# Kernel tuning notes

Hardware: AMD Instinct MI355X
Metric: run time of the kernel (lower is better)

Reference implementation:

```python
import jax, jax.numpy as jnp
import numpy as np

N, E = 50000, 640000
D_IN, D_OUT, N_BASES = 128, 128, 8


def setup_inputs() -> dict:
    key = jax.random.key(0)
    k1, k2, k3, k4, k5, k6 = jax.random.split(key, 6)
    x = jax.random.normal(k1, (N, D_IN), dtype=jnp.float32)
    edge_index = jax.random.randint(k2, (2, E), 0, N, dtype=jnp.int64)
    # basis-decomposed relation weights (num_relations=1)
    bases = jax.random.normal(k3, (N_BASES, D_IN, D_OUT), dtype=jnp.float32) * 0.05
    comp = jax.random.normal(k4, (1, N_BASES), dtype=jnp.float32)
    root = jax.random.normal(k5, (D_IN, D_OUT), dtype=jnp.float32) * 0.05
    bias = jax.random.normal(k6, (D_OUT,), dtype=jnp.float32) * 0.01
    return {"x": x, "edge_index": edge_index, "bases": bases,
            "comp": comp, "root": root, "bias": bias}


def reference(x, edge_index, bases, comp, root, bias):
    # W[rel=0] = sum_b comp[0,b] * bases[b]  -> [D_IN, D_OUT]
    W = jnp.einsum('b,bio->io', comp[0], bases)
    src = edge_index[0]  # message sources (x_j)
    dst = edge_index[1]  # aggregation targets
    # gather -> scatter-add (aggr='add'), then relation-specific transform
    agg = jax.ops.segment_sum(x[src], dst, num_segments=x.shape[0])  # [N, D_IN]
    out = agg @ W + x @ root + bias  # root/self-loop transform + bias
    return out
```

## Files before the change

### kernel.cpp

```cpp
#include <hip/hip_runtime.h>

#define N_NODES 50000
#define N_EDGES 640000
#define D 128
#define NB 8
#define PAD 64
#define BM 64
#define LDA 136

typedef _Float16 half_t;
typedef __attribute__((ext_vector_type(8))) _Float16 half8;
typedef __attribute__((ext_vector_type(4))) float f32x4;

__device__ __forceinline__ void add4(float4& acc, const float4& v) {
    acc.x += v.x; acc.y += v.y; acc.z += v.z; acc.w += v.w;
}

__global__ __launch_bounds__(256)
void compute_Wt_kernel(const float* __restrict__ bases,
                       const float* __restrict__ comp,
                       const float* __restrict__ root,
                       half_t* __restrict__ Wt,
                       half_t* __restrict__ Rt) {
    int idx = blockIdx.x * 256 + threadIdx.x;
    if (idx >= D * D) return;
    int i = idx >> 7, o = idx & 127;
    float acc = 0.f;
#pragma unroll
    for (int b = 0; b < NB; ++b)
        acc += comp[b] * bases[((size_t)b * D + i) * D + o];
    Wt[o * D + i] = (half_t)acc;
    Rt[o * D + i] = (half_t)root[idx];
}

__global__ __launch_bounds__(256)
void zero_cnt_kernel(int* __restrict__ cnt) {
    int i = blockIdx.x * 256 + threadIdx.x;
    if (i < N_NODES) cnt[i] = 0;
}

__global__ __launch_bounds__(256)
void gemm_mfma_kernel(const float* __restrict__ x,
                      const half_t* __restrict__ Wt,
                      const half_t* __restrict__ Rt,
                      const float* __restrict__ bias,
                      half_t* __restrict__ y,
                      float* __restrict__ out) {
    __shared__ __align__(16) half_t As[BM * LDA];
    const int row0 = blockIdx.x * BM;
    const int tid  = threadIdx.x;

    {
        int r  = tid >> 2;
        int cc = (tid & 3) * 32;
        if (row0 + r < N_NODES) {
            const float4* x4 = (const float4*)x;
            size_t base = (size_t)(row0 + r) * 32 + (cc >> 2);
#pragma unroll
            for (int u = 0; u < 4; ++u) {
                float4 v0 = x4[base + 2 * u];
                float4 v1 = x4[base + 2 * u + 1];
                half8 h;
                h[0] = (half_t)v0.x; h[1] = (half_t)v0.y;
                h[2] = (half_t)v0.z; h[3] = (half_t)v0.w;
                h[4] = (half_t)v1.x; h[5] = (half_t)v1.y;
                h[6] = (half_t)v1.z; h[7] = (half_t)v1.w;
                *(half8*)&As[r * LDA + cc + u * 8] = h;
            }
        }
    }
    __syncthreads();

    const int wave = tid >> 6;
    const int lane = tid & 63;
    const int m    = lane & 15;
    const int quad = lane >> 4;

    half8 a[4];
#pragma unroll
    for (int kk = 0; kk < 4; ++kk)
        a[kk] = *(const half8*)&As[(wave * 16 + m) * LDA + kk * 32 + quad * 8];

    f32x4 accW[8], accR[8];
#pragma unroll
    for (int nt = 0; nt < 8; ++nt) {
        accW[nt] = (f32x4){0.f, 0.f, 0.f, 0.f};
        accR[nt] = (f32x4){0.f, 0.f, 0.f, 0.f};
    }

#pragma unroll
    for (int nt = 0; nt < 8; ++nt) {
        const half_t* wp = Wt + (nt * 16 + m) * D + quad * 8;
        const half_t* rp = Rt + (nt * 16 + m) * D + quad * 8;
        half8 bw[4], br[4];
#pragma unroll
        for (int kk = 0; kk < 4; ++kk) {
            bw[kk] = *(const half8*)(wp + kk * 32);
            br[kk] = *(const half8*)(rp + kk * 32);
        }
#pragma unroll
        for (int kk = 0; kk < 4; ++kk) {
            accW[nt] = __builtin_amdgcn_mfma_f32_16x16x32_f16(a[kk], bw[kk], accW[nt], 0, 0, 0);
            accR[nt] = __builtin_amdgcn_mfma_f32_16x16x32_f16(a[kk], br[kk], accR[nt], 0, 0, 0);
        }
    }

#pragma unroll
    for (int nt = 0; nt < 8; ++nt) {
        int col = nt * 16 + m;
        float bb = bias[col];
#pragma unroll
        for (int r = 0; r < 4; ++r) {
            int row = row0 + wave * 16 + quad * 4 + r;
            if (row < N_NODES) {
                y[(size_t)row * D + col]   = (half_t)accW[nt][r];
                out[(size_t)row * D + col] = accR[nt][r] + bb;
            }
        }
    }
}

__global__ __launch_bounds__(256)
void bucket_kernel(const int* __restrict__ eidx,
                   const half_t* __restrict__ y,
                   float* __restrict__ out,
                   int* __restrict__ cnt,
                   int* __restrict__ bucket) {
    int e = blockIdx.x * 256 + threadIdx.x;
    if (e >= N_EDGES) return;
    int src = eidx[e];
    int dst = eidx[N_EDGES + e];
    int pos = atomicAdd(&cnt[dst], 1);
    if (pos < PAD) {
        bucket[(size_t)dst * PAD + pos] = src;
    } else {
        const half_t* yr = y + (size_t)src * D;
        float* op = out + (size_t)dst * D;
        for (int q = 0; q < D; ++q) atomicAdd(op + q, (float)yr[q]);
    }
}

__global__ __launch_bounds__(256)
void gather_kernel(const int* __restrict__ cnt,
                   const int* __restrict__ bucket,
                   const half_t* __restrict__ y,
                   float* __restrict__ out) {
    int node = blockIdx.x * 16 + (threadIdx.x >> 4);
    int q = threadIdx.x & 15;
    if (node >= N_NODES) return;
    int c = cnt[node];
    if (c > PAD) c = PAD;
    const int* b = bucket + (size_t)node * PAD;
    float acc[8] = {0.f, 0.f, 0.f, 0.f, 0.f, 0.f, 0.f, 0.f};
    int i = 0;
    for (; i + 4 <= c; i += 4) {
        int4 s = *(const int4*)(b + i);
        half8 v0 = *(const half8*)(y + (size_t)s.x * D + q * 8);
        half8 v1 = *(const half8*)(y + (size_t)s.y * D + q * 8);
        half8 v2 = *(const half8*)(y + (size_t)s.z * D + q * 8);
        half8 v3 = *(const half8*)(y + (size_t)s.w * D + q * 8);
#pragma unroll
        for (int j = 0; j < 8; ++j)
            acc[j] += (float)v0[j] + (float)v1[j] + (float)v2[j] + (float)v3[j];
    }
    for (; i < c; ++i) {
        half8 v = *(const half8*)(y + (size_t)b[i] * D + q * 8);
#pragma unroll
        for (int j = 0; j < 8; ++j) acc[j] += (float)v[j];
    }
    float4* op = (float4*)(out + (size_t)node * D + q * 8);
    float4 o0 = op[0], o1 = op[1];
    o0.x += acc[0]; o0.y += acc[1]; o0.z += acc[2]; o0.w += acc[3];
    o1.x += acc[4]; o1.y += acc[5]; o1.z += acc[6]; o1.w += acc[7];
    op[0] = o0; op[1] = o1;
}

extern "C" void kernel_launch(void* const* d_in, const int* in_sizes, int n_in,
                              void* d_out, int out_size, void* d_ws, size_t ws_size,
                              hipStream_t stream) {
    const float* x     = (const float*)d_in[0];
    const int*   eidx  = (const int*)d_in[1];
    const float* bases = (const float*)d_in[2];
    const float* comp  = (const float*)d_in[3];
    const float* root  = (const float*)d_in[4];
    const float* bias  = (const float*)d_in[5];
    float* out = (float*)d_out;

    char* ws = (char*)d_ws;
    half_t* y      = (half_t*)ws;
    half_t* Wt     = (half_t*)(ws + 12800000);
    half_t* Rt     = (half_t*)(ws + 12832768);
    int*    cnt    = (int*)(ws + 12865536);
    int*    bucket = (int*)(ws + 13065536);

    zero_cnt_kernel<<<(N_NODES + 255) / 256, 256, 0, stream>>>(cnt);
    compute_Wt_kernel<<<(D * D + 255) / 256, 256, 0, stream>>>(bases, comp, root, Wt, Rt);
    gemm_mfma_kernel<<<(N_NODES + BM - 1) / BM, 256, 0, stream>>>(x, Wt, Rt, bias, y, out);
    bucket_kernel<<<(N_EDGES + 255) / 256, 256, 0, stream>>>(eidx, y, out, cnt, bucket);
    gather_kernel<<<(N_NODES + 15) / 16, 256, 0, stream>>>(cnt, bucket, y, out);
}
```

Baseline: 183.5 us.

## Fuse GEMM with edge bucketing, merge init kernels, defer overflow edges

Merges the zero-count and weight-combine kernels into one init kernel, and runs the dense MFMA GEMM and the edge bucketing inside one launch by interleaving their blocks, so the latency-bound atomics overlap with the GEMM. Overflow edges beyond the per-node bucket capacity now go into a capped list that a separate drain kernel applies after gathering. The gather loop is also unrolled to eight neighbours per step. It adds a launch and risks silently dropping overflow edges past the cap, and mixing block types may cause imbalance.

```diff
diff --git a/kernel.cpp b/kernel.cpp
--- a/kernel.cpp
+++ b/kernel.cpp
@@ -7,136 +7,143 @@
 #define PAD 64
 #define BM 64
 #define LDA 136
+#define OVF_CAP 8192
+
+#define NT_G ((N_NODES + BM - 1) / BM)
+#define NT_B ((N_EDGES + 255) / 256)
 
 typedef _Float16 half_t;
 typedef __attribute__((ext_vector_type(8))) _Float16 half8;
 typedef __attribute__((ext_vector_type(4))) float f32x4;
 
-__device__ __forceinline__ void add4(float4& acc, const float4& v) {
-    acc.x += v.x; acc.y += v.y; acc.z += v.z; acc.w += v.w;
-}
-
-__global__ __launch_bounds__(256)
-void compute_Wt_kernel(const float* __restrict__ bases,
-                       const float* __restrict__ comp,
-                       const float* __restrict__ root,
-                       half_t* __restrict__ Wt,
-                       half_t* __restrict__ Rt) {
-    int idx = blockIdx.x * 256 + threadIdx.x;
-    if (idx >= D * D) return;
-    int i = idx >> 7, o = idx & 127;
-    float acc = 0.f;
-#pragma unroll
-    for (int b = 0; b < NB; ++b)
-        acc += comp[b] * bases[((size_t)b * D + i) * D + o];
-    Wt[o * D + i] = (half_t)acc;
-    Rt[o * D + i] = (half_t)root[idx];
-}
-
-__global__ __launch_bounds__(256)
-void zero_cnt_kernel(int* __restrict__ cnt) {
+__global__ __launch_bounds__(256)
+void init_kernel(const float* __restrict__ bases,
+                 const float* __restrict__ comp,
+                 const float* __restrict__ root,
+                 half_t* __restrict__ Wt,
+                 half_t* __restrict__ Rt,
+                 int* __restrict__ cnt,
+                 int* __restrict__ ovf_cnt) {
     int i = blockIdx.x * 256 + threadIdx.x;
+    if (i == 0) *ovf_cnt = 0;
     if (i < N_NODES) cnt[i] = 0;
-}
-
-__global__ __launch_bounds__(256)
-void gemm_mfma_kernel(const float* __restrict__ x,
-                      const half_t* __restrict__ Wt,
-                      const half_t* __restrict__ Rt,
-                      const float* __restrict__ bias,
-                      half_t* __restrict__ y,
-                      float* __restrict__ out) {
+    if (i < D * D) {
+        int ii = i >> 7, o = i & 127;
+        float acc = 0.f;
+#pragma unroll
+        for (int b = 0; b < NB; ++b)
+            acc += comp[b] * bases[((size_t)b * D + ii) * D + o];
+        Wt[o * D + ii] = (half_t)acc;
+        Rt[o * D + ii] = (half_t)root[i];
+    }
+}
+
+__global__ __launch_bounds__(256)
+void gemm_bucket_kernel(const float* __restrict__ x,
+                        const int* __restrict__ eidx,
+                        const half_t* __restrict__ Wt,
+                        const half_t* __restrict__ Rt,
+                        const float* __restrict__ bias,
+                        half_t* __restrict__ y,
+                        float* __restrict__ out,
+                        int* __restrict__ cnt,
+                        int* __restrict__ bucket,
+                        int* __restrict__ ovf_cnt,
+                        int2* __restrict__ ovf) {
     __shared__ __align__(16) half_t As[BM * LDA];
-    const int row0 = blockIdx.x * BM;
-    const int tid  = threadIdx.x;
-
-    {
-        int r  = tid >> 2;
-        int cc = (tid & 3) * 32;
-        if (row0 + r < N_NODES) {
-            const float4* x4 = (const float4*)x;
-            size_t base = (size_t)(row0 + r) * 32 + (cc >> 2);
-#pragma unroll
-            for (int u = 0; u < 4; ++u) {
-                float4 v0 = x4[base + 2 * u];
-                float4 v1 = x4[base + 2 * u + 1];
-                half8 h;
-                h[0] = (half_t)v0.x; h[1] = (half_t)v0.y;
-                h[2] = (half_t)v0.z; h[3] = (half_t)v0.w;
-                h[4] = (half_t)v1.x; h[5] = (half_t)v1.y;
-                h[6] = (half_t)v1.z; h[7] = (half_t)v1.w;
-                *(half8*)&As[r * LDA + cc + u * 8] = h;
-            }
-        }
-    }
-    __syncthreads();
-
-    const int wave = tid >> 6;
-    const int lane = tid & 63;
-    const int m    = lane & 15;
-    const int quad = lane >> 4;
-
-    half8 a[4];
-#pragma unroll
-    for (int kk = 0; kk < 4; ++kk)
-        a[kk] = *(const half8*)&As[(wave * 16 + m) * LDA + kk * 32 + quad * 8];
-
-    f32x4 accW[8], accR[8];
-#pragma unroll
-    for (int nt = 0; nt < 8; ++nt) {
-        accW[nt] = (f32x4){0.f, 0.f, 0.f, 0.f};
-        accR[nt] = (f32x4){0.f, 0.f, 0.f, 0.f};
-    }
-
-#pragma unroll
-    for (int nt = 0; nt < 8; ++nt) {
-        const half_t* wp = Wt + (nt * 16 + m) * D + quad * 8;
-        const half_t* rp = Rt + (nt * 16 + m) * D + quad * 8;
-        half8 bw[4], br[4];
-#pragma unroll
-        for (int kk = 0; kk < 4; ++kk) {
-            bw[kk] = *(const half8*)(wp + kk * 32);
-            br[kk] = *(const half8*)(rp + kk * 32);
-        }
-#pragma unroll
-        for (int kk = 0; kk < 4; ++kk) {
-            accW[nt] = __builtin_amdgcn_mfma_f32_16x16x32_f16(a[kk], bw[kk], accW[nt], 0, 0, 0);
-            accR[nt] = __builtin_amdgcn_mfma_f32_16x16x32_f16(a[kk], br[kk], accR[nt], 0, 0, 0);
-        }
-    }
-
-#pragma unroll
-    for (int nt = 0; nt < 8; ++nt) {
-        int col = nt * 16 + m;
-        float bb = bias[col];
-#pragma unroll
-        for (int r = 0; r < 4; ++r) {
-            int row = row0 + wave * 16 + quad * 4 + r;
-            if (row < N_NODES) {
-                y[(size_t)row * D + col]   = (half_t)accW[nt][r];
-                out[(size_t)row * D + col] = accR[nt][r] + bb;
-            }
-        }
-    }
-}
-
-__global__ __launch_bounds__(256)
-void bucket_kernel(const int* __restrict__ eidx,
-                   const half_t* __restrict__ y,
-                   float* __restrict__ out,
-                   int* __restrict__ cnt,
-                   int* __restrict__ bucket) {
-    int e = blockIdx.x * 256 + threadIdx.x;
-    if (e >= N_EDGES) return;
-    int src = eidx[e];
-    int dst = eidx[N_EDGES + e];
-    int pos = atomicAdd(&cnt[dst], 1);
-    if (pos < PAD) {
-        bucket[(size_t)dst * PAD + pos] = src;
+    const int tid = threadIdx.x;
+    const int t = blockIdx.x;
+
+    int gemm_tile = -1, bucket_tile = -1;
+    if (t < NT_G * 4) {
+        int g = t >> 2, r = t & 3;
+        if (r == 0) gemm_tile = g;
+        else        bucket_tile = g * 3 + (r - 1);
     } else {
-        const half_t* yr = y + (size_t)src * D;
-        float* op = out + (size_t)dst * D;
-        for (int q = 0; q < D; ++q) atomicAdd(op + q, (float)yr[q]);
+        bucket_tile = NT_G * 3 + (t - NT_G * 4);
+    }
+
+    if (gemm_tile >= 0) {
+        const int row0 = gemm_tile * BM;
+        {
+            int r  = tid >> 2;
+            int cc = (tid & 3) * 32;
+            if (row0 + r < N_NODES) {
+                const float4* x4 = (const float4*)x;
+                size_t base = (size_t)(row0 + r) * 32 + (cc >> 2);
+#pragma unroll
+                for (int u = 0; u < 4; ++u) {
+                    float4 v0 = x4[base + 2 * u];
+                    float4 v1 = x4[base + 2 * u + 1];
+                    half8 h;
+                    h[0] = (half_t)v0.x; h[1] = (half_t)v0.y;
+                    h[2] = (half_t)v0.z; h[3] = (half_t)v0.w;
+                    h[4] = (half_t)v1.x; h[5] = (half_t)v1.y;
+                    h[6] = (half_t)v1.z; h[7] = (half_t)v1.w;
+                    *(half8*)&As[r * LDA + cc + u * 8] = h;
+                }
+            }
+        }
+        __syncthreads();
+
+        const int wave = tid >> 6;
+        const int lane = tid & 63;
+        const int m    = lane & 15;
+        const int quad = lane >> 4;
+
+        half8 a[4];
+#pragma unroll
+        for (int kk = 0; kk < 4; ++kk)
+            a[kk] = *(const half8*)&As[(wave * 16 + m) * LDA + kk * 32 + quad * 8];
+
+        f32x4 accW[8], accR[8];
+#pragma unroll
+        for (int nt = 0; nt < 8; ++nt) {
+            accW[nt] = (f32x4){0.f, 0.f, 0.f, 0.f};
+            accR[nt] = (f32x4){0.f, 0.f, 0.f, 0.f};
+        }
+#pragma unroll
+        for (int nt = 0; nt < 8; ++nt) {
+            const half_t* wp = Wt + (nt * 16 + m) * D + quad * 8;
+            const half_t* rp = Rt + (nt * 16 + m) * D + quad * 8;
+            half8 bw[4], br[4];
+#pragma unroll
+            for (int kk = 0; kk < 4; ++kk) {
+                bw[kk] = *(const half8*)(wp + kk * 32);
+                br[kk] = *(const half8*)(rp + kk * 32);
+            }
+#pragma unroll
+            for (int kk = 0; kk < 4; ++kk) {
+                accW[nt] = __builtin_amdgcn_mfma_f32_16x16x32_f16(a[kk], bw[kk], accW[nt], 0, 0, 0);
+                accR[nt] = __builtin_amdgcn_mfma_f32_16x16x32_f16(a[kk], br[kk], accR[nt], 0, 0, 0);
+            }
+        }
+#pragma unroll
+        for (int nt = 0; nt < 8; ++nt) {
+            int col = nt * 16 + m;
+            float bb = bias[col];
+#pragma unroll
+            for (int r = 0; r < 4; ++r) {
+                int row = row0 + wave * 16 + quad * 4 + r;
+                if (row < N_NODES) {
+                    y[(size_t)row * D + col]   = (half_t)accW[nt][r];
+                    out[(size_t)row * D + col] = accR[nt][r] + bb;
+                }
+            }
+        }
+    } else {
+        int e = bucket_tile * 256 + tid;
+        if (e < N_EDGES) {
+            int src = eidx[e];
+            int dst = eidx[N_EDGES + e];
+            int pos = atomicAdd(&cnt[dst], 1);
+            if (pos < PAD) {
+                bucket[(size_t)dst * PAD + pos] = src;
+            } else {
+                int op = atomicAdd(ovf_cnt, 1);
+                if (op < OVF_CAP) ovf[op] = make_int2(dst, src);
+            }
+        }
     }
 }
 
@@ -153,6 +160,22 @@
     const int* b = bucket + (size_t)node * PAD;
     float acc[8] = {0.f, 0.f, 0.f, 0.f, 0.f, 0.f, 0.f, 0.f};
     int i = 0;
+    for (; i + 8 <= c; i += 8) {
+        int4 s0 = *(const int4*)(b + i);
+        int4 s1 = *(const int4*)(b + i + 4);
+        half8 v0 = *(const half8*)(y + (size_t)s0.x * D + q * 8);
+        half8 v1 = *(const half8*)(y + (size_t)s0.y * D + q * 8);
+        half8 v2 = *(const half8*)(y + (size_t)s0.z * D + q * 8);
+        half8 v3 = *(const half8*)(y + (size_t)s0.w * D + q * 8);
+        half8 v4 = *(const half8*)(y + (size_t)s1.x * D + q * 8);
+        half8 v5 = *(const half8*)(y + (size_t)s1.y * D + q * 8);
+        half8 v6 = *(const half8*)(y + (size_t)s1.z * D + q * 8);
+        half8 v7 = *(const half8*)(y + (size_t)s1.w * D + q * 8);
+#pragma unroll
+        for (int j = 0; j < 8; ++j)
+            acc[j] += ((float)v0[j] + (float)v1[j]) + ((float)v2[j] + (float)v3[j])
+                    + ((float)v4[j] + (float)v5[j]) + ((float)v6[j] + (float)v7[j]);
+    }
     for (; i + 4 <= c; i += 4) {
         int4 s = *(const int4*)(b + i);
         half8 v0 = *(const half8*)(y + (size_t)s.x * D + q * 8);
@@ -161,7 +184,7 @@
         half8 v3 = *(const half8*)(y + (size_t)s.w * D + q * 8);
 #pragma unroll
         for (int j = 0; j < 8; ++j)
-            acc[j] += (float)v0[j] + (float)v1[j] + (float)v2[j] + (float)v3[j];
+            acc[j] += ((float)v0[j] + (float)v1[j]) + ((float)v2[j] + (float)v3[j]);
     }
     for (; i < c; ++i) {
         half8 v = *(const half8*)(y + (size_t)b[i] * D + q * 8);
@@ -173,6 +196,21 @@
     o0.x += acc[0]; o0.y += acc[1]; o0.z += acc[2]; o0.w += acc[3];
     o1.x += acc[4]; o1.y += acc[5]; o1.z += acc[6]; o1.w += acc[7];
     op[0] = o0; op[1] = o1;
+}
+
+__global__ __launch_bounds__(256)
+void ovf_drain_kernel(const int* __restrict__ ovf_cnt,
+                      const int2* __restrict__ ovf,
+                      const half_t* __restrict__ y,
+                      float* __restrict__ out) {
+    int novf = *ovf_cnt;
+    if (novf > OVF_CAP) novf = OVF_CAP;
+    int total = novf * D;
+    for (int w = blockIdx.x * 256 + threadIdx.x; w < total; w += gridDim.x * 256) {
+        int e = w >> 7, qq = w & 127;
+        atomicAdd(out + (size_t)ovf[e].x * D + qq,
+                  (float)y[(size_t)ovf[e].y * D + qq]);
+    }
 }
 
 extern "C" void kernel_launch(void* const* d_in, const int* in_sizes, int n_in,
@@ -187,15 +225,18 @@
     float* out = (float*)d_out;
 
     char* ws = (char*)d_ws;
-    half_t* y      = (half_t*)ws;
-    half_t* Wt     = (half_t*)(ws + 12800000);
-    half_t* Rt     = (half_t*)(ws + 12832768);
-    int*    cnt    = (int*)(ws + 12865536);
-    int*    bucket = (int*)(ws + 13065536);
-
-    zero_cnt_kernel<<<(N_NODES + 255) / 256, 256, 0, stream>>>(cnt);
-    compute_Wt_kernel<<<(D * D + 255) / 256, 256, 0, stream>>>(bases, comp, root, Wt, Rt);
-    gemm_mfma_kernel<<<(N_NODES + BM - 1) / BM, 256, 0, stream>>>(x, Wt, Rt, bias, y, out);
-    bucket_kernel<<<(N_EDGES + 255) / 256, 256, 0, stream>>>(eidx, y, out, cnt, bucket);
+    half_t* y       = (half_t*)ws;
+    half_t* Wt      = (half_t*)(ws + 12800000);
+    half_t* Rt      = (half_t*)(ws + 12832768);
+    int*    cnt     = (int*)   (ws + 12865536);
+    int*    bucket  = (int*)   (ws + 13065536);
+    int*    ovf_cnt = (int*)   (ws + 25865536);
+    int2*   ovf     = (int2*)  (ws + 25865600);
+
+    init_kernel<<<(N_NODES + 255) / 256, 256, 0, stream>>>(
+        bases, comp, root, Wt, Rt, cnt, ovf_cnt);
+    gemm_bucket_kernel<<<NT_G * 4 + (NT_B - NT_G * 3), 256, 0, stream>>>(
+        x, eidx, Wt, Rt, bias, y, out, cnt, bucket, ovf_cnt, ovf);
     gather_kernel<<<(N_NODES + 15) / 16, 256, 0, stream>>>(cnt, bucket, y, out);
-}
+    ovf_drain_kernel<<<32, 256, 0, stream>>>(ovf_cnt, ovf, y, out);
+}
```

After: 245.2 us. 1.34x slower.
